# Kernel tuning notes

Hardware: AMD Instinct MI355X
Metric: run time of the kernel (lower is better)

The kernel has to match this reference:

```python
import jax, jax.numpy as jnp
import numpy as np

D_Z, D_X, K, T = 128, 64, 16, 2048
JITTER = 1e-4
# Tsit5 Butcher tableau. diffrax.diffeqsolve with the default ConstantStepSize
# controller and dt0 = t_curr - t_prev takes exactly ONE Tsit5 step per interval,
# so a single explicit Tsit5 step reproduces the original math.
A21 = 0.161
A31, A32 = -0.008480655492356989, 0.335480655492357
A41, A42, A43 = 2.8971530571054935, -6.359448489975075, 4.3622954328695815
A51, A52, A53, A54 = 5.325864828439257, -11.748883564062828, 7.4955393428898365, -0.09249506636175525
A61, A62, A63, A64, A65 = 5.86145544294642, -12.92096931784711, 8.159367898576159, -0.071584973281401, -0.028269050394068383
B1, B2, B3, B4, B5, B6 = 0.09646076681806523, 0.01, 0.4798896504144996, 1.379008574103742, -3.290069515436081, 2.324710524099774


def setup_inputs() -> dict:
    key = jax.random.key(0)
    ks = jax.random.split(key, 8)
    xs = jax.random.normal(ks[0], (T, D_X), jnp.float32)
    ts = jnp.arange(T, dtype=jnp.float32) * 0.01  # strictly increasing observation times
    expected_s = jax.nn.softmax(jax.random.normal(ks[1], (T, K), jnp.float32), axis=-1)
    mu_0 = jax.random.normal(ks[2], (D_Z,), jnp.float32)
    P_0 = jnp.eye(D_Z, dtype=jnp.float32)
    # stable continuous dynamics: small random part, negative diagonal shift
    A_s = 0.02 * jax.random.normal(ks[3], (K, D_Z, D_Z), jnp.float32) - 0.5 * jnp.eye(D_Z, dtype=jnp.float32)
    b_s = 0.1 * jax.random.normal(ks[4], (K, D_Z), jnp.float32)
    Q_s_chol = 0.1 + 0.1 * jax.random.uniform(ks[5], (K, D_Z), dtype=jnp.float32)
    C = jax.random.normal(ks[6], (D_X, D_Z), jnp.float32) / jnp.sqrt(jnp.float32(D_Z))
    R = 0.1 * jnp.eye(D_X, dtype=jnp.float32)
    return dict(xs=xs, ts=ts, expected_s=expected_s, mu_0=mu_0, P_0=P_0,
                A_s=A_s, b_s=b_s, Q_s_chol=Q_s_chol, C=C, R=R)


def _ode_func(state, s_prob, A_s, b_s, Q_s_chol):
    # state packs [mu (D_Z), P.flatten() (D_Z*D_Z)]
    mu, P = state[:D_Z], state[D_Z:].reshape(D_Z, D_Z)
    w = s_prob / jnp.sum(s_prob)  # jnp.average(..., weights=s_prob) semantics
    drift = jnp.einsum('k,kij,j->i', w, A_s, mu) + w @ b_s
    eA = jnp.einsum('k,kij->ij', w, A_s)
    eQ = jnp.diag(w @ (Q_s_chol ** 2))  # weighted avg of diag(Q_chol)^2
    dP = eA @ P + P @ eA.T + eQ
    return jnp.concatenate([drift, dP.reshape(-1)])


def _kf_update(mu, P, x, C, R):
    y = x - C @ mu
    S = C @ P @ C.T + R + JITTER * jnp.eye(R.shape[0], dtype=P.dtype)
    cho = jax.scipy.linalg.cho_factor(S)
    Kg = jax.scipy.linalg.cho_solve(cho, C @ P).T
    mu_u = mu + Kg @ y
    P_u = P - Kg @ C @ P
    return mu_u, 0.5 * (P_u + P_u.T)


def reference(xs, ts, expected_s, mu_0, P_0, A_s, b_s, Q_s_chol, C, R):
    mu0u, P0u = _kf_update(mu_0, P_0, xs[0], C, R)

    def step(carry, inp):
        mu_prev, P_prev, t_prev = carry
        x, t, s = inp
        y0 = jnp.concatenate([mu_prev, P_prev.reshape(-1)])
        f = lambda st: _ode_func(st, s, A_s, b_s, Q_s_chol)

        def integrate(_):
            h = t - t_prev
            k1 = f(y0)
            k2 = f(y0 + h * (A21 * k1))
            k3 = f(y0 + h * (A31 * k1 + A32 * k2))
            k4 = f(y0 + h * (A41 * k1 + A42 * k2 + A43 * k3))
            k5 = f(y0 + h * (A51 * k1 + A52 * k2 + A53 * k3 + A54 * k4))
            k6 = f(y0 + h * (A61 * k1 + A62 * k2 + A63 * k3 + A64 * k4 + A65 * k5))
            return y0 + h * (B1 * k1 + B2 * k2 + B3 * k3 + B4 * k4 + B5 * k5 + B6 * k6)

        state_pred = jax.lax.cond(t > t_prev, integrate, lambda _: y0, None)
        mu_pr, P_pr = state_pred[:D_Z], state_pred[D_Z:].reshape(D_Z, D_Z)
        mu_u, P_u = _kf_update(mu_pr, P_pr, x, C, R)
        return (mu_u, P_u, t), (mu_u, P_u)

    _, (mu_f, P_f) = jax.lax.scan(step, (mu0u, P0u, ts[0]), (xs[1:], ts[1:], expected_s[1:]))
    mu_filt = jnp.concatenate([mu0u[None], mu_f], axis=0)  # (T, D_Z)
    P_filt = jnp.concatenate([P0u[None], P_f], axis=0)  # (T, D_Z, D_Z)
    return mu_filt, P_filt
```

## Files before the change

### kernel.cpp

```cpp
#include <hip/hip_runtime.h>
#include <math.h>

#define DZ 128
#define DX 64
#define KMIX 16
#define JITTER_C 1e-4f
#define MS (DZ*DZ)
#define ESZ (4*MS + 2*DZ)
#define NCH 256
#define NT 1024
#define SCN (5*MS + 256)

#define SP   0
#define SX   (1*MS)
#define SX2  (2*MS)
#define SX2T (3*MS)
#define SQ   (4*MS)

template<int M, int N, int K, int MODE, bool DUAL>
__device__ void mm_(const float* __restrict__ At, const float* __restrict__ B,
                    float* __restrict__ out, const float* __restrict__ aux,
                    float* __restrict__ outT, float e1 = 0.f)
{
    __syncthreads();
    const int tid = threadIdx.x;
    constexpr int TM = M/32, TN = N/32;
    const int tx = tid & 31, ty = tid >> 5;
    const int i0 = ty*TM, j0 = tx*TN;
    float acc[TM*TN];
#pragma unroll
    for (int e = 0; e < TM*TN; ++e) acc[e] = 0.f;
#pragma unroll 4
    for (int k = 0; k < K; ++k) {
        const float* ar = At + k*M + i0;
        const float* br = B + k*N + j0;
        float av[TM], bv[TN];
        if constexpr (TM == 2) {
            float2 t = *reinterpret_cast<const float2*>(ar);
            av[0]=t.x; av[1]=t.y;
        } else {
#pragma unroll
            for (int a = 0; a < TM; a += 4) {
                float4 t = *reinterpret_cast<const float4*>(ar + a);
                av[a]=t.x; av[a+1]=t.y; av[a+2]=t.z; av[a+3]=t.w;
            }
        }
        if constexpr (TN == 2) {
            float2 t = *reinterpret_cast<const float2*>(br);
            bv[0]=t.x; bv[1]=t.y;
        } else {
#pragma unroll
            for (int b = 0; b < TN; b += 4) {
                float4 t = *reinterpret_cast<const float4*>(br + b);
                bv[b]=t.x; bv[b+1]=t.y; bv[b+2]=t.z; bv[b+3]=t.w;
            }
        }
#pragma unroll
        for (int a = 0; a < TM; ++a)
#pragma unroll
            for (int b = 0; b < TN; ++b)
                acc[a*TN+b] = fmaf(av[a], bv[b], acc[a*TN+b]);
    }
#pragma unroll
    for (int a = 0; a < TM; ++a) {
#pragma unroll
        for (int b = 0; b < TN; ++b) {
            const int row = i0+a, col = j0+b;
            const int idx = row*N + col;
            float v = acc[a*TN+b];
            if constexpr (MODE == 1) v += out[idx];
            else if constexpr (MODE == 2) v = aux[idx] - v;
            else if constexpr (MODE == 3) v += aux[idx];
            else if constexpr (MODE == 4) { v += e1*aux[idx]; if (row==col) v += 1.f; }
            out[idx] = v;
            acc[a*TN+b] = v;
        }
    }
    if constexpr (DUAL) {
#pragma unroll
        for (int b = 0; b < TN; ++b) {
#pragma unroll
            for (int a = 0; a < TM; a += 4) {
                float4 v = make_float4(acc[(a)*TN+b], acc[(a+1)*TN+b], acc[(a+2)*TN+b], acc[(a+3)*TN+b]);
                *reinterpret_cast<float4*>(outT + (j0+b)*M + i0 + a) = v;
            }
        }
    }
    __syncthreads();
}

template<int M, int K, int MODE>
__device__ void mv_(const float* __restrict__ At, const float* __restrict__ v,
                    float* __restrict__ out, const float* __restrict__ aux)
{
    __syncthreads();
    const int tid = threadIdx.x;
    if (tid < M) {
        float s = 0.f;
        for (int k = 0; k < K; ++k)
            s = fmaf(At[k*M + tid], v[k], s);
        float r;
        if constexpr (MODE == 0) r = s;
        else if constexpr (MODE == 1) r = aux[tid] + s;
        else r = aux[tid] - s;
        out[tid] = r;
    }
    __syncthreads();
}

__device__ void trans_g(const float* __restrict__ src, float* __restrict__ dst,
                        float* __restrict__ Lb)
{
    __syncthreads();
    for (int e = threadIdx.x; e < MS; e += NT) Lb[e] = src[e];
    __syncthreads();
    for (int e = threadIdx.x; e < MS; e += NT) {
        int j = e >> 7, i = e & 127;
        dst[e] = Lb[i*DZ + j];
    }
    __syncthreads();
}

__device__ void gj64_spd(float* __restrict__ A, float* __restrict__ pc, float* __restrict__ pr)
{
    __syncthreads();
    const int tid = threadIdx.x;
    for (int p = 0; p < DX; ++p) {
        if (tid < DX) { pc[tid] = A[tid*DX + p]; pr[tid] = A[p*DX + tid]; }
        __syncthreads();
        const float rp = 1.f / pr[p];
        for (int e = tid; e < DX*DX; e += NT) {
            const int i = e >> 6, j = e & 63;
            const float pv = pr[j] * rp;
            float o;
            if (i == p) o = (j == p) ? rp : pv;
            else { const float fc = pc[i]; o = (j == p) ? (-fc*rp) : (A[e] - fc*pv); }
            A[e] = o;
        }
        __syncthreads();
    }
}

__device__ void gj128_piv(float* __restrict__ A, float* __restrict__ pc, float* __restrict__ pr,
                          int* __restrict__ rec, int* __restrict__ ipv1)
{
    __syncthreads();
    const int tid = threadIdx.x;
    for (int p = 0; p < DZ; ++p) {
        if (tid < 64) {
            float best = -1.f; int bi = p;
            for (int i = tid; i < DZ; i += 64) {
                float v = (i >= p) ? fabsf(A[i*DZ + p]) : -2.f;
                if (v > best) { best = v; bi = i; }
            }
            for (int off = 32; off > 0; off >>= 1) {
                float ob = __shfl_xor(best, off);
                int obi = __shfl_xor(bi, off);
                if (ob > best) { best = ob; bi = obi; }
            }
            if (tid == 0) { rec[p] = bi; ipv1[0] = bi; }
        }
        __syncthreads();
        const int r = ipv1[0];
        if (r != p) {
            for (int j = tid; j < DZ; j += NT) { float t = A[p*DZ+j]; A[p*DZ+j] = A[r*DZ+j]; A[r*DZ+j] = t; }
            __syncthreads();
        }
        if (tid < DZ) { pc[tid] = A[tid*DZ + p]; pr[tid] = A[p*DZ + tid]; }
        __syncthreads();
        const float rp = 1.f / pr[p];
        for (int e = tid; e < MS; e += NT) {
            const int i = e >> 7, j = e & 127;
            const float pv = pr[j] * rp;
            float o;
            if (i == p) o = (j == p) ? rp : pv;
            else { const float fc = pc[i]; o = (j == p) ? (-fc*rp) : (A[e] - fc*pv); }
            A[e] = o;
        }
        __syncthreads();
    }
    for (int p = DZ - 1; p >= 0; --p) {
        const int r = rec[p];
        if (r != p) {
            for (int i = tid; i < DZ; i += NT) { float t = A[i*DZ+p]; A[i*DZ+p] = A[i*DZ+r]; A[i*DZ+r] = t; }
            __syncthreads();
        }
    }
    __syncthreads();
}

__device__ void phase1_dev(int k,
    const float* __restrict__ A_s, const float* __restrict__ b_s,
    const float* __restrict__ Qch, const float* __restrict__ es, const float* __restrict__ ts,
    float* sx, float* sx2, float* sx2t, float* sq,
    float* L0, float* L1,
    float* W16, float* ebv, float* eqv, float* vvv, float* cvec,
    float g1, float g2, float g3, float g4)
{
    const int tid = threadIdx.x;
    const float h = ts[k] - ts[k-1];
    if (h <= 0.f) {
        __syncthreads();
        for (int e = tid; e < MS; e += NT) {
            int i = e >> 7, j = e & 127;
            L0[e] = (i==j) ? 1.f : 0.f;
            sq[e] = 0.f;
        }
        if (tid < DZ) cvec[tid] = 0.f;
        __syncthreads();
        return;
    }
    __syncthreads();
    if (tid < KMIX) W16[tid] = es[(size_t)k*KMIX + tid];
    __syncthreads();
    if (tid == 0) {
        float s = 0.f;
        for (int m = 0; m < KMIX; ++m) s += W16[m];
        float inv = 1.f/s;
        for (int m = 0; m < KMIX; ++m) W16[m] *= inv;
    }
    __syncthreads();
    if (tid < DZ) {
        float eb = 0.f, eq = 0.f;
        for (int m = 0; m < KMIX; ++m) {
            float wm = W16[m];
            eb = fmaf(wm, b_s[m*DZ+tid], eb);
            float qc = Qch[m*DZ+tid];
            eq = fmaf(wm, qc*qc, eq);
        }
        ebv[tid] = eb; eqv[tid] = eq;
    }
    const int tx = tid & 31, ty = tid >> 5;
    const int i0 = ty*4, j0 = tx*4;
    float t16[16];
#pragma unroll
    for (int e = 0; e < 16; ++e) t16[e] = 0.f;
    for (int m = 0; m < KMIX; ++m) {
        float wm = W16[m];
        const float* Am = A_s + (size_t)m * MS;
#pragma unroll
        for (int a = 0; a < 4; ++a) {
            float4 p0 = *reinterpret_cast<const float4*>(&Am[(i0+a)*DZ + j0]);
            t16[a*4+0]=fmaf(wm,p0.x,t16[a*4+0]); t16[a*4+1]=fmaf(wm,p0.y,t16[a*4+1]);
            t16[a*4+2]=fmaf(wm,p0.z,t16[a*4+2]); t16[a*4+3]=fmaf(wm,p0.w,t16[a*4+3]);
        }
    }
#pragma unroll
    for (int a = 0; a < 4; ++a)
#pragma unroll
        for (int b = 0; b < 4; ++b) {
            float v = h * t16[a*4+b];
            L1[(i0+a)*DZ + (j0+b)] = v;
            sx[(i0+a)*DZ + (j0+b)] = v;
            L0[(j0+b)*DZ + (i0+a)] = v;
        }
    __syncthreads();
    {
        float gg[5]; gg[1]=g1; gg[2]=g2; gg[3]=g3; gg[4]=g4;
        if (tid < DZ) vvv[tid] = ebv[tid];
        float creg = (tid < DZ) ? g1 * ebv[tid] : 0.f;
        __syncthreads();
        for (int m = 1; m <= 3; ++m) {
            float vn = 0.f;
            if (tid < DZ)
                for (int kk = 0; kk < DZ; ++kk)
                    vn = fmaf(L0[kk*DZ + tid], vvv[kk], vn);
            __syncthreads();
            if (tid < DZ) vvv[tid] = vn;
            creg = fmaf(gg[m+1], vn, creg);
            __syncthreads();
        }
        if (tid < DZ) cvec[tid] = h * creg;
    }
    mm_<128,128,128,0,true>(L0, L1, sx2, nullptr, sx2t);
    for (int e = tid; e < MS; e += NT) {
        int j = e >> 7, i = e & 127;
        float xt = L0[e];
        float w1  = g2*sx[e] + g3*sx2[e];
        float w1t = g2*xt    + g3*sx2t[e];
        float vq = w1*eqv[i] + eqv[j]*w1t;
        if (i == j) vq += g1*eqv[j];
        sq[e] = h * vq;
        L1[e] = g3*xt + ((i==j) ? g2 : 0.f);
    }
    __syncthreads();
    mm_<128,128,128,4,false>(sx2, L1, L0, L0, nullptr, g1);
}

#define SHARED_DECLS \
    __shared__ __align__(16) float L0[MS]; \
    __shared__ __align__(16) float L1[MS]; \
    __shared__ __align__(16) float SL[DX*DX]; \
    __shared__ float V0[DZ],V1[DZ],V2[DZ],V3[DZ],V4[DZ],V5[DZ]; \
    __shared__ float r64s[DX], u64s[DX]; \
    __shared__ float W16[KMIX], ebv[DZ], eqv[DZ], vvv[DZ], cvec[DZ]; \
    __shared__ float GJc[DZ], GJr[DZ]; \
    __shared__ int REC[DZ]; __shared__ int IPV1[1];

__global__ __launch_bounds__(NT) void kf_prep(
    const float* __restrict__ Cm, const float* __restrict__ Rm,
    const float* __restrict__ mu0, const float* __restrict__ P0,
    const float* __restrict__ xs,
    float* Ct, float* Rj, float* Rji, float* mu0u, float* p0u, float* scr)
{
    SHARED_DECLS
    const int tid = threadIdx.x;
    for (int i = tid; i < DZ*DX; i += NT) { int z = i>>6, m = i&63; Ct[i] = Cm[m*DZ + z]; }
    for (int i = tid; i < DX*DX; i += NT) {
        int a = i>>6, b = i&63;
        float v = Rm[i] + ((a==b) ? JITTER_C : 0.f);
        Rj[i] = v; SL[i] = v;
    }
    gj64_spd(SL, GJc, GJr);
    for (int i = tid; i < DX*DX; i += NT) Rji[i] = SL[i];
    float* z  = scr + SX;
    float* cp = scr + SX + DZ*DX;
    float* kt = scr + SX2;
    mm_<128,64,128,0,true>(P0, Ct, z, nullptr, cp);
    mm_<64,64,128,3,false>(Ct, z, SL, Rj, nullptr);
    gj64_spd(SL, GJc, GJr);
    mm_<64,128,64,0,false>(SL, cp, kt, nullptr, nullptr);
    mv_<64,128,2>(Ct, mu0, r64s, xs);
    mv_<128,64,1>(kt, r64s, mu0u, mu0);
    mm_<128,128,64,2,false>(kt, cp, p0u, P0, nullptr);
    __syncthreads();
    for (int e = tid; e < MS; e += NT) L0[e] = p0u[e];
    __syncthreads();
    for (int e = tid; e < MS; e += NT) {
        int i = e>>7, j = e&127;
        p0u[e] = 0.5f * (L0[e] + L0[j*DZ + i]);
    }
}

__global__ __launch_bounds__(NT) void kf_passA(
    const float* __restrict__ A_s, const float* __restrict__ b_s,
    const float* __restrict__ Qch, const float* __restrict__ es,
    const float* __restrict__ ts, const float* __restrict__ xs,
    const float* __restrict__ Ct, const float* __restrict__ Rj,
    const float* __restrict__ Rji,
    const float* __restrict__ mu0u, const float* __restrict__ p0u,
    float* elems, float* scr, int T, int LCH,
    float g1, float g2, float g3, float g4)
{
    SHARED_DECLS
    const int c = blockIdx.x, tid = threadIdx.x;
    float* sc = scr + (size_t)c * SCN;
    float* R = elems + (size_t)c * ESZ;
    float* RAs = R; float* RAts = R+MS; float* RCs = R+2*MS; float* RJs = R+3*MS;
    float* Rbs = R+4*MS; float* Rhs = R+4*MS+DZ;
    int eBeg = c*LCH, eEnd = (c*LCH + LCH < T) ? (c*LCH + LCH) : T;
    if (eBeg >= eEnd && c != 0) {
        for (int e = tid; e < MS; e += NT) {
            int i = e>>7, j = e&127; float id = (i==j)?1.f:0.f;
            RAs[e]=id; RAts[e]=id; RCs[e]=0.f; RJs[e]=0.f;
        }
        if (tid < DZ) { Rbs[tid]=0.f; Rhs[tid]=0.f; }
        return;
    }
    if (c == 0) {
        for (int e = tid; e < MS; e += NT) { RAs[e]=0.f; RCs[e]=p0u[e]; RJs[e]=0.f; }
        if (tid < DZ) { V0[tid]=mu0u[tid]; V5[tid]=0.f; }
        eBeg = 1;
    } else {
        for (int e = tid; e < MS; e += NT) {
            int i = e>>7, j = e&127;
            RAs[e] = (i==j)?1.f:0.f; RCs[e]=0.f; RJs[e]=0.f;
        }
        if (tid < DZ) { V0[tid]=0.f; V5[tid]=0.f; }
    }
    __syncthreads();
    float* sx = sc+SX; float* sx2 = sc+SX2; float* sx2t = sc+SX2T; float* sq = sc+SQ;
    float* z  = sx2t;  float* zt = sx2t + 8192;
    float* y  = sq;    float* hh = sq + 8192;
    float* h2 = sx;
    for (int e = eBeg; e < eEnd; ++e) {
        phase1_dev(e, A_s,b_s,Qch,es,ts, sx,sx2,sx2t,sq, L0,L1,
                   W16,ebv,eqv,vvv,cvec, g1,g2,g3,g4);
        mm_<128,128,128,0,false>(L0, RAs, sx, nullptr, nullptr);
        mv_<128,128,1>(L0, V0, V1, cvec);
        mm_<128,128,128,0,false>(RCs, L0, sx2, nullptr, nullptr);
        mm_<128,128,128,3,false>(L0, sx2, L1, sq, nullptr);
        mm_<128,64,128,0,true>(L1, Ct, z, nullptr, zt);
        mm_<64,64,128,3,false>(Ct, z, SL, Rj, nullptr);
        gj64_spd(SL, GJc, GJr);
        mm_<64,128,128,0,false>(Ct, sx, y, nullptr, nullptr);
        mm_<64,128,64,0,false>(SL, y, hh, nullptr, nullptr);
        mm_<128,128,64,2,false>(zt, hh, RAs, sx, nullptr);
        mm_<128,128,64,1,false>(y, hh, RJs, nullptr, nullptr);
        mm_<64,128,64,0,false>(SL, zt, h2, nullptr, nullptr);
        mm_<128,128,64,2,false>(zt, h2, RCs, L1, nullptr);
        mv_<64,128,2>(Ct, V1, r64s, xs + (size_t)e*DX);
        mv_<64,64,0>(Rji, xs + (size_t)e*DX, u64s, nullptr);
        mv_<128,64,1>(zt, u64s, V2, V1);
        mv_<64,128,0>(Ct, V2, GJc, nullptr);
        mv_<64,64,0>(SL, GJc, GJr, nullptr);
        mv_<128,64,2>(zt, GJr, V0, V2);
        mv_<64,64,0>(SL, r64s, u64s, nullptr);
        mv_<128,64,1>(y, u64s, V5, V5);
    }
    __syncthreads();
    if (tid < DZ) { Rbs[tid] = V0[tid]; Rhs[tid] = V5[tid]; }
    trans_g(RAs, RAts, L0);
}

__device__ void combine(float* Rd,
    const float* EA, const float* EAt, const float* EC, const float* EJ,
    const float* Ebg, const float* Ehg,
    float* t1, float* t2, float* t3,
    float* L0, float* L1,
    float* V0, float* V1, float* V2, float* V3, float* V4, float* V5,
    float* GJc, float* GJr, int* REC, int* IPV1, int lastj)
{
    float* RA = Rd; float* RAt = Rd+MS; float* RC = Rd+2*MS; float* RJ = Rd+3*MS;
    float* Rb = Rd+4*MS; float* Rh = Rd+4*MS+DZ;
    const int tid = threadIdx.x;
    __syncthreads();
    if (tid < DZ) { V0[tid]=Ebg[tid]; V1[tid]=Ehg[tid]; V2[tid]=Rb[tid]; }
    mm_<128,128,128,0,false>(EJ, RC, L0, nullptr, nullptr);
    if (tid < DZ) L0[tid*DZ + tid] += 1.f;
    gj128_piv(L0, GJc, GJr, REC, IPV1);
    if (!lastj) {
        mm_<128,128,128,0,false>(L0, RA, t1, nullptr, nullptr);
        mm_<128,128,128,0,false>(EJ, RA, t2, nullptr, nullptr);
        mm_<128,128,128,1,false>(t1, t2, RJ, nullptr, nullptr);
        mv_<128,128,2>(EJ, V2, V4, V1);
        mv_<128,128,1>(t1, V4, Rh, Rh);
    }
    mv_<128,128,1>(RC, V1, V3, V2);
    mv_<128,128,0>(L0, V3, V5, nullptr);
    mv_<128,128,1>(EAt, V5, Rb, V0);
    mm_<128,128,128,0,false>(L0, RC, t3, nullptr, nullptr);
    mm_<128,128,128,0,false>(t3, EAt, t2, nullptr, nullptr);
    mm_<128,128,128,3,false>(EAt, t2, RC, EC, nullptr);
    if (!lastj) {
        mm_<128,128,128,0,false>(EAt, t1, RA, nullptr, nullptr);
        trans_g(RA, RAt, L1);
    }
}

__global__ __launch_bounds__(NT) void kf_scan(
    const float* __restrict__ in, float* __restrict__ out, float* scr, int r, int lastj)
{
    SHARED_DECLS
    const int c = blockIdx.x;
    float* sc = scr + (size_t)c * SCN;
    float* dst = out + (size_t)c * ESZ;
    const float* src = in + (size_t)((c >= r) ? (c - r) : c) * ESZ;
    if (lastj) {
        for (int e = threadIdx.x; e < MS; e += NT) dst[2*MS + e] = src[2*MS + e];
        for (int e = threadIdx.x; e < DZ; e += NT) dst[4*MS + e] = src[4*MS + e];
    } else {
        for (int e = threadIdx.x; e < ESZ; e += NT) dst[e] = src[e];
    }
    if (c >= r) {
        const float* E = in + (size_t)c * ESZ;
        combine(dst, E, E+MS, E+2*MS, E+3*MS, E+4*MS, E+4*MS+DZ,
                sc+SP, sc+SX, sc+SX2, L0, L1,
                V0,V1,V2,V3,V4,V5, GJc, GJr, REC, IPV1, lastj);
    }
}

__global__ __launch_bounds__(NT) void kf_passC(
    const float* __restrict__ A_s, const float* __restrict__ b_s,
    const float* __restrict__ Qch, const float* __restrict__ es,
    const float* __restrict__ ts, const float* __restrict__ xs,
    const float* __restrict__ Ct, const float* __restrict__ Rj,
    const float* __restrict__ mu0u, const float* __restrict__ p0u,
    const float* __restrict__ pfx,
    float* mu_out, float* P_out, float* scr, int T, int LCH,
    float g1, float g2, float g3, float g4)
{
    SHARED_DECLS
    const int c = blockIdx.x, tid = threadIdx.x;
    float* sc = scr + (size_t)c * SCN;
    float* P = sc + SP;
    int eBeg = c*LCH, eEnd = (c*LCH + LCH < T) ? (c*LCH + LCH) : T;
    if (eBeg >= eEnd && c != 0) return;
    if (c == 0) {
        for (int e = tid; e < MS; e += NT) { float v = p0u[e]; P[e] = v; P_out[e] = v; }
        if (tid < DZ) { V0[tid] = mu0u[tid]; mu_out[tid] = mu0u[tid]; }
        eBeg = 1;
    } else {
        const float* X = pfx + (size_t)(c-1) * ESZ;
        for (int e = tid; e < MS; e += NT) P[e] = X[2*MS + e];
        if (tid < DZ) V0[tid] = X[4*MS + tid];
    }
    __syncthreads();
    float* sx = sc+SX; float* sx2 = sc+SX2; float* sx2t = sc+SX2T; float* sq = sc+SQ;
    float* z  = sx2t;  float* zt = sx2t + 8192;
    for (int e = eBeg; e < eEnd; ++e) {
        phase1_dev(e, A_s,b_s,Qch,es,ts, sx,sx2,sx2t,sq, L0,L1,
                   W16,ebv,eqv,vvv,cvec, g1,g2,g3,g4);
        mm_<128,128,128,0,false>(P, L0, sx, nullptr, nullptr);
        mm_<128,128,128,3,false>(L0, sx, sx2, sq, nullptr);
        mv_<128,128,1>(L0, V0, V1, cvec);
        mm_<128,64,128,0,true>(sx2, Ct, z, nullptr, zt);
        mm_<64,64,128,3,false>(Ct, z, SL, Rj, nullptr);
        gj64_spd(SL, GJc, GJr);
        mm_<64,128,64,0,false>(SL, zt, sq, nullptr, nullptr);
        mv_<64,128,2>(Ct, V1, r64s, xs + (size_t)e*DX);
        mv_<128,64,1>(sq, r64s, V0, V1);
        if (tid < DZ) mu_out[(size_t)e*DZ + tid] = V0[tid];
        mm_<128,128,64,2,false>(zt, sq, L1, sx2, nullptr);
        float* po = P_out + (size_t)e * MS;
        for (int ee = tid; ee < MS; ee += NT) {
            int i = ee>>7, j = ee&127;
            float v = 0.5f * (L1[ee] + L1[j*DZ + i]);
            P[ee] = v; po[ee] = v;
        }
        __syncthreads();
    }
}

static void compute_gamma(double g[7])
{
    const double A[6][5] = {
        {0, 0, 0, 0, 0},
        {0.161, 0, 0, 0, 0},
        {-0.008480655492356989, 0.335480655492357, 0, 0, 0},
        {2.8971530571054935, -6.359448489975075, 4.3622954328695815, 0, 0},
        {5.325864828439257, -11.748883564062828, 7.4955393428898365, -0.09249506636175525, 0},
        {5.86145544294642, -12.92096931784711, 8.159367898576159, -0.071584973281401, -0.028269050394068383}};
    const double B[6] = {0.09646076681806523, 0.01, 0.4798896504144996,
                         1.379008574103742, -3.290069515436081, 2.324710524099774};
    double e[6][6];
    for (int i = 0; i < 6; ++i)
        for (int d = 0; d < 6; ++d) e[i][d] = 0.0;
    for (int i = 0; i < 6; ++i) {
        e[i][0] = 1.0;
        for (int j = 0; j < i; ++j)
            for (int d = 0; d < 5; ++d)
                e[i][d + 1] += A[i][j] * e[j][d];
    }
    g[0] = 1.0;
    for (int m = 1; m <= 6; ++m) {
        double s = 0.0;
        for (int i = 0; i < 6; ++i) s += B[i] * e[i][m - 1];
        g[m] = s;
    }
}

extern "C" void kernel_launch(void* const* d_in, const int* in_sizes, int n_in,
                              void* d_out, int out_size, void* d_ws, size_t ws_size,
                              hipStream_t stream)
{
    const float* xs  = (const float*)d_in[0];
    const float* ts  = (const float*)d_in[1];
    const float* es  = (const float*)d_in[2];
    const float* mu0 = (const float*)d_in[3];
    const float* P0  = (const float*)d_in[4];
    const float* A_s = (const float*)d_in[5];
    const float* b_s = (const float*)d_in[6];
    const float* Qch = (const float*)d_in[7];
    const float* Cm  = (const float*)d_in[8];
    const float* Rm  = (const float*)d_in[9];
    const int T = in_sizes[1];

    float* mu_out = (float*)d_out;
    float* P_out  = mu_out + (size_t)T * DZ;

    float* ws = (float*)d_ws;
    float* Ct    = ws;
    float* Rj    = ws + 8192;
    float* Rji   = ws + 12288;
    float* mu0u  = ws + 16384;
    float* p0u   = ws + 16512;
    float* elemsA = ws + 32896;
    float* elemsB = elemsA + (size_t)NCH * ESZ;
    float* scr    = elemsB + (size_t)NCH * ESZ;

    const int LCH = (T + NCH - 1) / NCH;

    double g[7];
    compute_gamma(g);
    const float g1 = (float)g[1], g2 = (float)g[2], g3 = (float)g[3], g4 = (float)g[4];

    hipLaunchKernelGGL(kf_prep, dim3(1), dim3(NT), 0, stream,
                       Cm, Rm, mu0, P0, xs, Ct, Rj, Rji, mu0u, p0u, scr);
    hipLaunchKernelGGL(kf_passA, dim3(NCH), dim3(NT), 0, stream,
                       A_s, b_s, Qch, es, ts, xs, Ct, Rj, Rji, mu0u, p0u,
                       elemsA, scr, T, LCH, g1, g2, g3, g4);
    float* bufs[2] = {elemsA, elemsB};
    int cur = 0;
    for (int r = 1; r < NCH; r <<= 1) {
        const int lastj = ((r << 1) >= NCH) ? 1 : 0;
        hipLaunchKernelGGL(kf_scan, dim3(NCH), dim3(NT), 0, stream,
                           bufs[cur], bufs[cur ^ 1], scr, r, lastj);
        cur ^= 1;
    }
    hipLaunchKernelGGL(kf_passC, dim3(NCH), dim3(NT), 0, stream,
                       A_s, b_s, Qch, es, ts, xs, Ct, Rj, mu0u, p0u,
                       bufs[cur], mu_out, P_out, scr, T, LCH, g1, g2, g3, g4);
}
```

Measured before the change: 13.17 ms.

## Block the 64x64 Gauss-Jordan inverse by 4 and keep intermediates in shared memory

Rewrites the 64x64 SPD Gauss-Jordan inversion to eliminate four pivots per sweep. Each thread inverts the 4x4 pivot block locally and applies a rank-4 update, cutting the number of barrier-separated passes by a factor of four. Several per-step intermediates (z/zt, t1, the Joseph-form product) are moved from global scratch into shared L0/L1 buffers. The P_out writes now use nontemporal stores, and the matmul k-loop unroll is raised from 4 to 8. Blocked elimination without pivoting relies on the SPD structure and may change rounding slightly, and buffer reuse of L0/L1 must not overlap live data.

```diff
diff --git a/kernel.cpp b/kernel.cpp
--- a/kernel.cpp
+++ b/kernel.cpp
@@ -30,7 +30,7 @@
     float acc[TM*TN];
 #pragma unroll
     for (int e = 0; e < TM*TN; ++e) acc[e] = 0.f;
-#pragma unroll 4
+#pragma unroll 8
     for (int k = 0; k < K; ++k) {
         const float* ar = At + k*M + i0;
         const float* br = B + k*N + j0;
@@ -121,24 +121,66 @@
     __syncthreads();
 }
 
-__device__ void gj64_spd(float* __restrict__ A, float* __restrict__ pc, float* __restrict__ pr)
-{
-    __syncthreads();
+__device__ void gj64_spd(float* __restrict__ A, float* __restrict__ st)
+{
     const int tid = threadIdx.x;
-    for (int p = 0; p < DX; ++p) {
-        if (tid < DX) { pc[tid] = A[tid*DX + p]; pr[tid] = A[p*DX + tid]; }
-        __syncthreads();
-        const float rp = 1.f / pr[p];
+    for (int p = 0; p < DX; p += 4) {
+        __syncthreads();
+        if (tid < 64) {
+#pragma unroll
+            for (int b = 0; b < 4; ++b) st[tid*4+b] = A[tid*DX + p + b];
+        } else if (tid < 128) {
+            int j = tid - 64;
+#pragma unroll
+            for (int b = 0; b < 4; ++b) st[256 + b*64 + j] = A[(p+b)*DX + j];
+        }
+        __syncthreads();
+        float Dm[16], Di[16];
+#pragma unroll
+        for (int a = 0; a < 4; ++a)
+#pragma unroll
+            for (int b = 0; b < 4; ++b) {
+                Dm[a*4+b] = st[(p+a)*4 + b];
+                Di[a*4+b] = (a==b) ? 1.f : 0.f;
+            }
+#pragma unroll
+        for (int q = 0; q < 4; ++q) {
+            float rp = 1.f / Dm[q*4+q];
+#pragma unroll
+            for (int j = 0; j < 4; ++j) { Dm[q*4+j] *= rp; Di[q*4+j] *= rp; }
+#pragma unroll
+            for (int i = 0; i < 4; ++i) {
+                if (i == q) continue;
+                float f = Dm[i*4+q];
+#pragma unroll
+                for (int j = 0; j < 4; ++j) { Dm[i*4+j] = fmaf(-f, Dm[q*4+j], Dm[i*4+j]); Di[i*4+j] = fmaf(-f, Di[q*4+j], Di[i*4+j]); }
+            }
+        }
         for (int e = tid; e < DX*DX; e += NT) {
             const int i = e >> 6, j = e & 63;
-            const float pv = pr[j] * rp;
+            const bool iP = (i >= p) && (i < p+4);
+            const bool jP = (j >= p) && (j < p+4);
             float o;
-            if (i == p) o = (j == p) ? rp : pv;
-            else { const float fc = pc[i]; o = (j == p) ? (-fc*rp) : (A[e] - fc*pv); }
+            if (iP && jP) {
+                o = Di[(i-p)*4 + (j-p)];
+            } else if (iP) {
+                const int a = i - p;
+                o = Di[a*4+0]*st[256+0*64+j] + Di[a*4+1]*st[256+1*64+j]
+                  + Di[a*4+2]*st[256+2*64+j] + Di[a*4+3]*st[256+3*64+j];
+            } else {
+                float Ei[4];
+#pragma unroll
+                for (int b = 0; b < 4; ++b)
+                    Ei[b] = st[i*4+0]*Di[0*4+b] + st[i*4+1]*Di[1*4+b]
+                          + st[i*4+2]*Di[2*4+b] + st[i*4+3]*Di[3*4+b];
+                if (jP) o = -Ei[j-p];
+                else    o = A[e] - (Ei[0]*st[256+0*64+j] + Ei[1]*st[256+1*64+j]
+                                  + Ei[2]*st[256+2*64+j] + Ei[3]*st[256+3*64+j]);
+            }
             A[e] = o;
         }
-        __syncthreads();
-    }
+    }
+    __syncthreads();
 }
 
 __device__ void gj128_piv(float* __restrict__ A, float* __restrict__ pc, float* __restrict__ pr,
@@ -291,6 +333,7 @@
     __shared__ __align__(16) float L0[MS]; \
     __shared__ __align__(16) float L1[MS]; \
     __shared__ __align__(16) float SL[DX*DX]; \
+    __shared__ __align__(16) float GJB[520]; \
     __shared__ float V0[DZ],V1[DZ],V2[DZ],V3[DZ],V4[DZ],V5[DZ]; \
     __shared__ float r64s[DX], u64s[DX]; \
     __shared__ float W16[KMIX], ebv[DZ], eqv[DZ], vvv[DZ], cvec[DZ]; \
@@ -311,14 +354,14 @@
         float v = Rm[i] + ((a==b) ? JITTER_C : 0.f);
         Rj[i] = v; SL[i] = v;
     }
-    gj64_spd(SL, GJc, GJr);
+    gj64_spd(SL, GJB);
     for (int i = tid; i < DX*DX; i += NT) Rji[i] = SL[i];
     float* z  = scr + SX;
     float* cp = scr + SX + DZ*DX;
     float* kt = scr + SX2;
     mm_<128,64,128,0,true>(P0, Ct, z, nullptr, cp);
     mm_<64,64,128,3,false>(Ct, z, SL, Rj, nullptr);
-    gj64_spd(SL, GJc, GJr);
+    gj64_spd(SL, GJB);
     mm_<64,128,64,0,false>(SL, cp, kt, nullptr, nullptr);
     mv_<64,128,2>(Ct, mu0, r64s, xs);
     mv_<128,64,1>(kt, r64s, mu0u, mu0);
@@ -370,7 +413,7 @@
     }
     __syncthreads();
     float* sx = sc+SX; float* sx2 = sc+SX2; float* sx2t = sc+SX2T; float* sq = sc+SQ;
-    float* z  = sx2t;  float* zt = sx2t + 8192;
+    float* z  = L0;    float* zt = L0 + 8192;
     float* y  = sq;    float* hh = sq + 8192;
     float* h2 = sx;
     for (int e = eBeg; e < eEnd; ++e) {
@@ -382,7 +425,7 @@
         mm_<128,128,128,3,false>(L0, sx2, L1, sq, nullptr);
         mm_<128,64,128,0,true>(L1, Ct, z, nullptr, zt);
         mm_<64,64,128,3,false>(Ct, z, SL, Rj, nullptr);
-        gj64_spd(SL, GJc, GJr);
+        gj64_spd(SL, GJB);
         mm_<64,128,128,0,false>(Ct, sx, y, nullptr, nullptr);
         mm_<64,128,64,0,false>(SL, y, hh, nullptr, nullptr);
         mm_<128,128,64,2,false>(zt, hh, RAs, sx, nullptr);
@@ -406,7 +449,7 @@
 __device__ void combine(float* Rd,
     const float* EA, const float* EAt, const float* EC, const float* EJ,
     const float* Ebg, const float* Ehg,
-    float* t1, float* t2, float* t3,
+    float* t2, float* t3,
     float* L0, float* L1,
     float* V0, float* V1, float* V2, float* V3, float* V4, float* V5,
     float* GJc, float* GJr, int* REC, int* IPV1, int lastj)
@@ -420,11 +463,11 @@
     if (tid < DZ) L0[tid*DZ + tid] += 1.f;
     gj128_piv(L0, GJc, GJr, REC, IPV1);
     if (!lastj) {
-        mm_<128,128,128,0,false>(L0, RA, t1, nullptr, nullptr);
+        mm_<128,128,128,0,false>(L0, RA, L1, nullptr, nullptr);
         mm_<128,128,128,0,false>(EJ, RA, t2, nullptr, nullptr);
-        mm_<128,128,128,1,false>(t1, t2, RJ, nullptr, nullptr);
+        mm_<128,128,128,1,false>(L1, t2, RJ, nullptr, nullptr);
         mv_<128,128,2>(EJ, V2, V4, V1);
-        mv_<128,128,1>(t1, V4, Rh, Rh);
+        mv_<128,128,1>(L1, V4, Rh, Rh);
     }
     mv_<128,128,1>(RC, V1, V3, V2);
     mv_<128,128,0>(L0, V3, V5, nullptr);
@@ -433,7 +476,7 @@
     mm_<128,128,128,0,false>(t3, EAt, t2, nullptr, nullptr);
     mm_<128,128,128,3,false>(EAt, t2, RC, EC, nullptr);
     if (!lastj) {
-        mm_<128,128,128,0,false>(EAt, t1, RA, nullptr, nullptr);
+        mm_<128,128,128,0,false>(EAt, L1, RA, nullptr, nullptr);
         trans_g(RA, RAt, L1);
     }
 }
@@ -455,7 +498,7 @@
     if (c >= r) {
         const float* E = in + (size_t)c * ESZ;
         combine(dst, E, E+MS, E+2*MS, E+3*MS, E+4*MS, E+4*MS+DZ,
-                sc+SP, sc+SX, sc+SX2, L0, L1,
+                sc+SP, sc+SX, L0, L1,
                 V0,V1,V2,V3,V4,V5, GJc, GJr, REC, IPV1, lastj);
     }
 }
@@ -487,26 +530,27 @@
     }
     __syncthreads();
     float* sx = sc+SX; float* sx2 = sc+SX2; float* sx2t = sc+SX2T; float* sq = sc+SQ;
-    float* z  = sx2t;  float* zt = sx2t + 8192;
+    float* z  = L0;    float* zt = L0 + 8192;
     for (int e = eBeg; e < eEnd; ++e) {
         phase1_dev(e, A_s,b_s,Qch,es,ts, sx,sx2,sx2t,sq, L0,L1,
                    W16,ebv,eqv,vvv,cvec, g1,g2,g3,g4);
         mm_<128,128,128,0,false>(P, L0, sx, nullptr, nullptr);
-        mm_<128,128,128,3,false>(L0, sx, sx2, sq, nullptr);
+        mm_<128,128,128,3,false>(L0, sx, L1, sq, nullptr);
         mv_<128,128,1>(L0, V0, V1, cvec);
-        mm_<128,64,128,0,true>(sx2, Ct, z, nullptr, zt);
+        mm_<128,64,128,0,true>(L1, Ct, z, nullptr, zt);
         mm_<64,64,128,3,false>(Ct, z, SL, Rj, nullptr);
-        gj64_spd(SL, GJc, GJr);
-        mm_<64,128,64,0,false>(SL, zt, sq, nullptr, nullptr);
+        gj64_spd(SL, GJB);
+        mm_<64,128,64,0,false>(SL, zt, sx2, nullptr, nullptr);
         mv_<64,128,2>(Ct, V1, r64s, xs + (size_t)e*DX);
-        mv_<128,64,1>(sq, r64s, V0, V1);
+        mv_<128,64,1>(sx2, r64s, V0, V1);
         if (tid < DZ) mu_out[(size_t)e*DZ + tid] = V0[tid];
-        mm_<128,128,64,2,false>(zt, sq, L1, sx2, nullptr);
+        mm_<128,128,64,2,false>(zt, sx2, L1, L1, nullptr);
         float* po = P_out + (size_t)e * MS;
         for (int ee = tid; ee < MS; ee += NT) {
             int i = ee>>7, j = ee&127;
             float v = 0.5f * (L1[ee] + L1[j*DZ + i]);
-            P[ee] = v; po[ee] = v;
+            P[ee] = v;
+            __builtin_nontemporal_store(v, &po[ee]);
         }
         __syncthreads();
     }
```

Measured after the change: 11.93 ms. 9.4% less time.
